# Optimization experiments

Hardware: AMD Instinct MI355X
Metric: run time of the kernel (lower is better)

The kernel has to match this reference:

```python
import jax, jax.numpy as jnp
import numpy as np

GROUP_SIZE = 128
IN_FEATURES = 8192
OUT_FEATURES = 28672
TOKENS = 32


def _dequantize(qweight, qzeros, scales):
    """ExLlama q4 dequant.
    qweight: (K//8, N) int32, 8 int4 values per word packed along k.
    qzeros:  (G, N//8) int32, 8 int4 zeros per word packed along n.
    scales:  (G, N) fp16.  g = k // GROUP_SIZE; w = s * (q - (z + 1)).
    """
    shifts = jnp.arange(8, dtype=jnp.int32) * 4
    K = qweight.shape[0] * 8
    N = qweight.shape[1]
    G = qzeros.shape[0]
    # unpack weights along k: (K//8, 8, N) -> (K, N)
    q = (qweight[:, None, :] >> shifts[None, :, None]) & 15
    q = q.reshape(K, N)
    # unpack zeros along n: (G, N//8, 8) -> (G, N)
    z = (qzeros[:, :, None] >> shifts[None, None, :]) & 15
    z = z.reshape(G, N)
    # group-wise dequant: reshape k into (G, GROUP_SIZE)
    qg = q.reshape(G, GROUP_SIZE, N).astype(jnp.float16)
    zf = (z + 1).astype(jnp.float16)[:, None, :]          # ExLlama stores zero-1
    w = (qg - zf) * scales[:, None, :]                    # (G, GS, N) fp16
    return w.reshape(K, N)


def setup_inputs() -> dict:
    key = jax.random.key(0)
    k1, k2, k3, k4, k5 = jax.random.split(key, 5)
    x = jax.random.normal(k1, (TOKENS, IN_FEATURES), dtype=jnp.float16)
    qweight = jax.random.randint(k2, (IN_FEATURES // 8, OUT_FEATURES),
                                 minval=-(2**31), maxval=2**31 - 1, dtype=jnp.int32)
    qzeros = jax.random.randint(k3, (IN_FEATURES // GROUP_SIZE, OUT_FEATURES // 8),
                                minval=-(2**31), maxval=2**31 - 1, dtype=jnp.int32)
    scales = (jax.random.uniform(k4, (IN_FEATURES // GROUP_SIZE, OUT_FEATURES),
                                 dtype=jnp.float32) * 0.01 + 0.001).astype(jnp.float16)
    bias = jax.random.normal(k5, (OUT_FEATURES,), dtype=jnp.float16)
    return {"x": x, "qweight": qweight, "qzeros": qzeros,
            "scales": scales, "bias": bias}


def reference(x, qweight, qzeros, scales, bias):
    w = _dequantize(qweight, qzeros, scales)              # (K, N) fp16
    out = jnp.matmul(x.astype(jnp.float16), w)            # (T, N)
    return out + bias
```

## Files before the change

kernel.cpp:

```cpp
#include <hip/hip_runtime.h>

#define T_TOK   32
#define KDIM    8192
#define NDIM    28672
#define NZW     3584
#define NSEG    16
#define SEGK    (KDIM / NSEG)
#define GPS     4
#define XIT     ((T_TOK * SEGK) / (256 * 8))

typedef _Float16 half8  __attribute__((ext_vector_type(8)));
typedef float    f32x4  __attribute__((ext_vector_type(4)));
typedef _Float16 half2v __attribute__((ext_vector_type(2)));
typedef unsigned uint4v __attribute__((ext_vector_type(4)));

template<bool ATOMIC>
__global__ __launch_bounds__(256)
void exllama_gemm16(const int*   __restrict__ qweight,
                    const int*   __restrict__ qzeros,
                    const float* __restrict__ scales,
                    const float* __restrict__ x,
                    const float* __restrict__ bias,
                    _Float16*    __restrict__ ws,
                    float*       __restrict__ out)
{
    __shared__ alignas(16) _Float16 xs[T_TOK * SEGK];
    char* xb = (char*)xs;

    const int tid  = threadIdx.x;
    const int lane = tid & 63;
    const int wav  = tid >> 6;
    const int quad = lane >> 4;
    const int l16  = lane & 15;
    const int seg  = blockIdx.y;
    const int n0   = blockIdx.x * 128 + wav * 32;
    const int g0   = seg * GPS;

    int nc[2];
    #pragma unroll
    for (int j = 0; j < 2; ++j) nc[j] = n0 + j * 16 + l16;

    unsigned qw[GPS][8];
    #pragma unroll
    for (int g = 0; g < GPS; ++g) {
        const size_t rb = (size_t)((g0 + g) * 16 + quad) * NDIM;
        #pragma unroll
        for (int c = 0; c < 4; ++c)
            #pragma unroll
            for (int j = 0; j < 2; ++j)
                qw[g][c * 2 + j] = (unsigned)qweight[rb + (size_t)(c * 4) * NDIM + nc[j]];
    }

    float sraw[GPS][2];
    int   zraw[GPS][2];
    #pragma unroll
    for (int g = 0; g < GPS; ++g)
        #pragma unroll
        for (int j = 0; j < 2; ++j) {
            sraw[g][j] = scales[(size_t)(g0 + g) * NDIM + nc[j]];
            zraw[g][j] = qzeros[(size_t)(g0 + g) * NZW + (nc[j] >> 3)];
        }

    {
        const int kseg0 = seg * SEGK;
        #pragma unroll
        for (int it = 0; it < XIT; ++it) {
            const int e  = it * 2048 + tid * 8;
            const int t  = e >> 9;
            const int kl = e & (SEGK - 1);
            const float* xp = x + (size_t)t * KDIM + kseg0 + kl;
            f32x4 lo = *(const f32x4*)xp;
            f32x4 hi = *(const f32x4*)(xp + 4);
            uint4v u;
            #pragma unroll
            for (int j = 0; j < 4; ++j)
                u[j] = __builtin_bit_cast(unsigned,
                          __builtin_amdgcn_cvt_pkrtz(lo[j], hi[j]));
            const int off = (t * 1024 + kl * 2) ^ ((t & 7) << 4);
            *(uint4v*)(xb + off) = u;
        }
    }

    half2v sp[GPS][2], cp[GPS][2];
    #pragma unroll
    for (int g = 0; g < GPS; ++g)
        #pragma unroll
        for (int j = 0; j < 2; ++j) {
            const int z = (zraw[g][j] >> ((nc[j] & 7) * 4)) & 15;
            const _Float16 sh = (_Float16)sraw[g][j];
            const _Float16 ch = (_Float16)(float)(-(1025 + z));
            sp[g][j] = (half2v){sh, sh};
            cp[g][j] = (half2v){ch, ch};
        }

    __syncthreads();

    f32x4 acc[2][2];
    #pragma unroll
    for (int j = 0; j < 2; ++j)
        #pragma unroll
        for (int m = 0; m < 2; ++m)
            acc[j][m] = (f32x4){0.f, 0.f, 0.f, 0.f};

    #pragma unroll
    for (int g = 0; g < GPS; ++g) {
        #pragma unroll
        for (int c = 0; c < 4; ++c) {
            const int kloc = g * 128 + c * 32 + quad * 8;
            const int o0 = (l16 * 1024 + kloc * 2) ^ ((l16 & 7) << 4);
            half8 a0 = *(const half8*)(xb + o0);
            half8 a1 = *(const half8*)(xb + o0 + 16 * 1024);
            #pragma unroll
            for (int j = 0; j < 2; ++j) {
                const unsigned w = qw[g][c * 2 + j];
                uint4v bu;
                #pragma unroll
                for (int i = 0; i < 4; ++i) {
                    unsigned t = ((w >> (4 * i)) & 0x000F000Fu) | 0x64006400u;
                    half2v th = __builtin_bit_cast(half2v, t);
                    half2v r  = (th + cp[g][j]) * sp[g][j];
                    bu[i] = __builtin_bit_cast(unsigned, r);
                }
                half8 bf = __builtin_bit_cast(half8, bu);
                acc[j][0] = __builtin_amdgcn_mfma_f32_16x16x32_f16(a0, bf, acc[j][0], 0, 0, 0);
                acc[j][1] = __builtin_amdgcn_mfma_f32_16x16x32_f16(a1, bf, acc[j][1], 0, 0, 0);
            }
        }
    }

    if (ATOMIC) {
        #pragma unroll
        for (int j = 0; j < 2; ++j) {
            const float bb = bias[nc[j]] * (1.0f / NSEG);
            #pragma unroll
            for (int m = 0; m < 2; ++m)
                #pragma unroll
                for (int r = 0; r < 4; ++r) {
                    const int t = m * 16 + quad * 4 + r;
                    unsafeAtomicAdd(out + (size_t)t * NDIM + nc[j], acc[j][m][r] + bb);
                }
        }
    } else {
        _Float16* wsp = ws + (size_t)seg * (T_TOK * NDIM);
        #pragma unroll
        for (int j = 0; j < 2; ++j)
            #pragma unroll
            for (int m = 0; m < 2; ++m)
                #pragma unroll
                for (int r = 0; r < 4; ++r) {
                    const int t = m * 16 + quad * 4 + r;
                    wsp[(size_t)t * NDIM + nc[j]] = (_Float16)acc[j][m][r];
                }
    }
}

__global__ __launch_bounds__(256)
void reduce_bias(const _Float16* __restrict__ ws,
                 const float*    __restrict__ bias,
                 float*          __restrict__ out)
{
    const int e = (blockIdx.x * 256 + threadIdx.x) * 8;
    const int n = e % NDIM;
    float sum[8] = {0.f, 0.f, 0.f, 0.f, 0.f, 0.f, 0.f, 0.f};
    #pragma unroll
    for (int s = 0; s < NSEG; ++s) {
        half8 v = *(const half8*)(ws + (size_t)s * (T_TOK * NDIM) + e);
        #pragma unroll
        for (int i = 0; i < 8; ++i) sum[i] += (float)v[i];
    }
    f32x4 o0, o1;
    #pragma unroll
    for (int i = 0; i < 4; ++i) {
        o0[i] = sum[i]     + bias[n + i];
        o1[i] = sum[i + 4] + bias[n + 4 + i];
    }
    *(f32x4*)(out + e)     = o0;
    *(f32x4*)(out + e + 4) = o1;
}

extern "C" void kernel_launch(void* const* d_in, const int* in_sizes, int n_in,
                              void* d_out, int out_size, void* d_ws, size_t ws_size,
                              hipStream_t stream)
{
    const float* x  = (const float*)d_in[0];
    const int* qweight = (const int*)d_in[1];
    const int* qzeros  = (const int*)d_in[2];
    const float* sc = (const float*)d_in[3];
    const float* bs = (const float*)d_in[4];
    float* out      = (float*)d_out;

    const size_t need = (size_t)NSEG * T_TOK * NDIM * sizeof(_Float16);
    if (ws_size >= need) {
        exllama_gemm16<false><<<dim3(NDIM / 128, NSEG), 256, 0, stream>>>(
            qweight, qzeros, sc, x, bs, (_Float16*)d_ws, out);
        reduce_bias<<<(T_TOK * NDIM) / (256 * 8), 256, 0, stream>>>(
            (const _Float16*)d_ws, bs, out);
    } else {
        exllama_gemm16<true><<<dim3(NDIM / 128, NSEG), 256, 0, stream>>>(
            qweight, qzeros, sc, x, bs, nullptr, out);
    }
}
```

Measured before the change: 198.3 us.

## Precompute fp16 activations once and read them directly from global memory

Adds a separate pre-pass kernel that converts x from fp32 to fp16 once into workspace. The GEMM kernel then drops its shared-memory staging and barrier and loads MFMA A-fragments straight from global memory (L2-resident), prefetching the next fragment one step ahead. This removes the per-block redundant conversion, the LDS traffic and the __syncthreads, which also frees LDS to allow higher occupancy. The cost is an extra kernel launch and uncoalesced, repeated global reads of x that depend on cache hits.

```diff
diff --git a/kernel.cpp b/kernel.cpp
--- a/kernel.cpp
+++ b/kernel.cpp
@@ -7,26 +7,36 @@
 #define NSEG    16
 #define SEGK    (KDIM / NSEG)
 #define GPS     4
-#define XIT     ((T_TOK * SEGK) / (256 * 8))
 
 typedef _Float16 half8  __attribute__((ext_vector_type(8)));
+typedef _Float16 half2v __attribute__((ext_vector_type(2)));
 typedef float    f32x4  __attribute__((ext_vector_type(4)));
-typedef _Float16 half2v __attribute__((ext_vector_type(2)));
 typedef unsigned uint4v __attribute__((ext_vector_type(4)));
 
-template<bool ATOMIC>
 __global__ __launch_bounds__(256)
-void exllama_gemm16(const int*   __restrict__ qweight,
-                    const int*   __restrict__ qzeros,
-                    const float* __restrict__ scales,
-                    const float* __restrict__ x,
-                    const float* __restrict__ bias,
-                    _Float16*    __restrict__ ws,
-                    float*       __restrict__ out)
-{
-    __shared__ alignas(16) _Float16 xs[T_TOK * SEGK];
-    char* xb = (char*)xs;
-
+void xprep(const float* __restrict__ x, _Float16* __restrict__ xp)
+{
+    const int idx = blockIdx.x * 256 + threadIdx.x;
+    const int t   = idx >> 10;
+    const int k0  = (idx & 1023) * 8;
+    const float* src = x + (size_t)t * KDIM + k0;
+    f32x4 lo = *(const f32x4*)src;
+    f32x4 hi = *(const f32x4*)(src + 4);
+    uint4v u;
+    #pragma unroll
+    for (int j = 0; j < 4; ++j)
+        u[j] = __builtin_bit_cast(unsigned,
+                  __builtin_amdgcn_cvt_pkrtz(lo[j], hi[j]));
+    *(uint4v*)(xp + (size_t)t * KDIM + k0) = u;
+}
+
+__global__ __launch_bounds__(256)
+void exllama_gemm_nolds(const int*      __restrict__ qweight,
+                        const int*      __restrict__ qzeros,
+                        const float*    __restrict__ scales,
+                        const _Float16* __restrict__ xp,
+                        _Float16*       __restrict__ ws)
+{
     const int tid  = threadIdx.x;
     const int lane = tid & 63;
     const int wav  = tid >> 6;
@@ -35,10 +45,11 @@
     const int seg  = blockIdx.y;
     const int n0   = blockIdx.x * 128 + wav * 32;
     const int g0   = seg * GPS;
+    const int kseg0 = seg * SEGK;
 
     int nc[2];
-    #pragma unroll
-    for (int j = 0; j < 2; ++j) nc[j] = n0 + j * 16 + l16;
+    nc[0] = n0 + l16;
+    nc[1] = n0 + 16 + l16;
 
     unsigned qw[GPS][8];
     #pragma unroll
@@ -61,25 +72,8 @@
             zraw[g][j] = qzeros[(size_t)(g0 + g) * NZW + (nc[j] >> 3)];
         }
 
-    {
-        const int kseg0 = seg * SEGK;
-        #pragma unroll
-        for (int it = 0; it < XIT; ++it) {
-            const int e  = it * 2048 + tid * 8;
-            const int t  = e >> 9;
-            const int kl = e & (SEGK - 1);
-            const float* xp = x + (size_t)t * KDIM + kseg0 + kl;
-            f32x4 lo = *(const f32x4*)xp;
-            f32x4 hi = *(const f32x4*)(xp + 4);
-            uint4v u;
-            #pragma unroll
-            for (int j = 0; j < 4; ++j)
-                u[j] = __builtin_bit_cast(unsigned,
-                          __builtin_amdgcn_cvt_pkrtz(lo[j], hi[j]));
-            const int off = (t * 1024 + kl * 2) ^ ((t & 7) << 4);
-            *(uint4v*)(xb + off) = u;
-        }
-    }
+    const _Float16* xr0 = xp + (size_t)l16 * KDIM + kseg0 + quad * 8;
+    const _Float16* xr1 = xr0 + (size_t)16 * KDIM;
 
     half2v sp[GPS][2], cp[GPS][2];
     #pragma unroll
@@ -93,8 +87,6 @@
             cp[g][j] = (half2v){ch, ch};
         }
 
-    __syncthreads();
-
     f32x4 acc[2][2];
     #pragma unroll
     for (int j = 0; j < 2; ++j)
@@ -102,6 +94,155 @@
         for (int m = 0; m < 2; ++m)
             acc[j][m] = (f32x4){0.f, 0.f, 0.f, 0.f};
 
+    half8 a0 = *(const half8*)(xr0);
+    half8 a1 = *(const half8*)(xr1);
+    #pragma unroll
+    for (int g = 0; g < GPS; ++g) {
+        #pragma unroll
+        for (int c = 0; c < 4; ++c) {
+            const half8 ca0 = a0;
+            const half8 ca1 = a1;
+            const int nx = g * 4 + c + 1;
+            if (nx < 16) {
+                const int kn = (nx >> 2) * 128 + (nx & 3) * 32;
+                a0 = *(const half8*)(xr0 + kn);
+                a1 = *(const half8*)(xr1 + kn);
+            }
+            #pragma unroll
+            for (int j = 0; j < 2; ++j) {
+                const unsigned w = qw[g][c * 2 + j];
+                uint4v bu;
+                #pragma unroll
+                for (int i = 0; i < 4; ++i) {
+                    unsigned t = ((w >> (4 * i)) & 0x000F000Fu) | 0x64006400u;
+                    half2v th = __builtin_bit_cast(half2v, t);
+                    half2v r  = (th + cp[g][j]) * sp[g][j];
+                    bu[i] = __builtin_bit_cast(unsigned, r);
+                }
+                half8 bf = __builtin_bit_cast(half8, bu);
+                acc[j][0] = __builtin_amdgcn_mfma_f32_16x16x32_f16(ca0, bf, acc[j][0], 0, 0, 0);
+                acc[j][1] = __builtin_amdgcn_mfma_f32_16x16x32_f16(ca1, bf, acc[j][1], 0, 0, 0);
+            }
+        }
+    }
+
+    _Float16* wsp = ws + (size_t)seg * (T_TOK * NDIM);
+    #pragma unroll
+    for (int j = 0; j < 2; ++j)
+        #pragma unroll
+        for (int m = 0; m < 2; ++m)
+            #pragma unroll
+            for (int r = 0; r < 4; ++r) {
+                const int t = m * 16 + quad * 4 + r;
+                wsp[(size_t)t * NDIM + nc[j]] = (_Float16)acc[j][m][r];
+            }
+}
+
+__global__ __launch_bounds__(256)
+void reduce_bias(const _Float16* __restrict__ ws,
+                 const float*    __restrict__ bias,
+                 float*          __restrict__ out)
+{
+    const int e = (blockIdx.x * 256 + threadIdx.x) * 8;
+    const int n = e % NDIM;
+    float sum[8] = {0.f, 0.f, 0.f, 0.f, 0.f, 0.f, 0.f, 0.f};
+    #pragma unroll
+    for (int s = 0; s < NSEG; ++s) {
+        half8 v = *(const half8*)(ws + (size_t)s * (T_TOK * NDIM) + e);
+        #pragma unroll
+        for (int i = 0; i < 8; ++i) sum[i] += (float)v[i];
+    }
+    f32x4 o0, o1;
+    #pragma unroll
+    for (int i = 0; i < 4; ++i) {
+        o0[i] = sum[i]     + bias[n + i];
+        o1[i] = sum[i + 4] + bias[n + 4 + i];
+    }
+    *(f32x4*)(out + e)     = o0;
+    *(f32x4*)(out + e + 4) = o1;
+}
+
+__global__ __launch_bounds__(256)
+void exllama_gemm_atomic(const int*   __restrict__ qweight,
+                         const int*   __restrict__ qzeros,
+                         const float* __restrict__ scales,
+                         const float* __restrict__ x,
+                         const float* __restrict__ bias,
+                         float*       __restrict__ out)
+{
+    __shared__ alignas(16) _Float16 xs[T_TOK * SEGK];
+    char* xb = (char*)xs;
+
+    const int tid  = threadIdx.x;
+    const int lane = tid & 63;
+    const int wav  = tid >> 6;
+    const int quad = lane >> 4;
+    const int l16  = lane & 15;
+    const int seg  = blockIdx.y;
+    const int n0   = blockIdx.x * 128 + wav * 32;
+    const int g0   = seg * GPS;
+
+    int nc[2];
+    nc[0] = n0 + l16;
+    nc[1] = n0 + 16 + l16;
+
+    unsigned qw[GPS][8];
+    #pragma unroll
+    for (int g = 0; g < GPS; ++g) {
+        const size_t rb = (size_t)((g0 + g) * 16 + quad) * NDIM;
+        #pragma unroll
+        for (int c = 0; c < 4; ++c)
+            #pragma unroll
+            for (int j = 0; j < 2; ++j)
+                qw[g][c * 2 + j] = (unsigned)qweight[rb + (size_t)(c * 4) * NDIM + nc[j]];
+    }
+    float sraw[GPS][2];
+    int   zraw[GPS][2];
+    #pragma unroll
+    for (int g = 0; g < GPS; ++g)
+        #pragma unroll
+        for (int j = 0; j < 2; ++j) {
+            sraw[g][j] = scales[(size_t)(g0 + g) * NDIM + nc[j]];
+            zraw[g][j] = qzeros[(size_t)(g0 + g) * NZW + (nc[j] >> 3)];
+        }
+    {
+        const int kseg0 = seg * SEGK;
+        #pragma unroll
+        for (int it = 0; it < 8; ++it) {
+            const int e  = it * 2048 + tid * 8;
+            const int t  = e >> 9;
+            const int kl = e & (SEGK - 1);
+            const float* xpr = x + (size_t)t * KDIM + kseg0 + kl;
+            f32x4 lo = *(const f32x4*)xpr;
+            f32x4 hi = *(const f32x4*)(xpr + 4);
+            uint4v u;
+            #pragma unroll
+            for (int j = 0; j < 4; ++j)
+                u[j] = __builtin_bit_cast(unsigned,
+                          __builtin_amdgcn_cvt_pkrtz(lo[j], hi[j]));
+            const int off = (t * 1024 + kl * 2) ^ ((t & 7) << 4);
+            *(uint4v*)(xb + off) = u;
+        }
+    }
+    half2v sp[GPS][2], cp[GPS][2];
+    #pragma unroll
+    for (int g = 0; g < GPS; ++g)
+        #pragma unroll
+        for (int j = 0; j < 2; ++j) {
+            const int z = (zraw[g][j] >> ((nc[j] & 7) * 4)) & 15;
+            const _Float16 sh = (_Float16)sraw[g][j];
+            const _Float16 ch = (_Float16)(float)(-(1025 + z));
+            sp[g][j] = (half2v){sh, sh};
+            cp[g][j] = (half2v){ch, ch};
+        }
+    __syncthreads();
+
+    f32x4 acc[2][2];
+    #pragma unroll
+    for (int j = 0; j < 2; ++j)
+        #pragma unroll
+        for (int m = 0; m < 2; ++m)
+            acc[j][m] = (f32x4){0.f, 0.f, 0.f, 0.f};
     #pragma unroll
     for (int g = 0; g < GPS; ++g) {
         #pragma unroll
@@ -127,55 +268,17 @@
             }
         }
     }
-
-    if (ATOMIC) {
-        #pragma unroll
-        for (int j = 0; j < 2; ++j) {
-            const float bb = bias[nc[j]] * (1.0f / NSEG);
-            #pragma unroll
-            for (int m = 0; m < 2; ++m)
-                #pragma unroll
-                for (int r = 0; r < 4; ++r) {
-                    const int t = m * 16 + quad * 4 + r;
-                    unsafeAtomicAdd(out + (size_t)t * NDIM + nc[j], acc[j][m][r] + bb);
-                }
-        }
-    } else {
-        _Float16* wsp = ws + (size_t)seg * (T_TOK * NDIM);
-        #pragma unroll
-        for (int j = 0; j < 2; ++j)
-            #pragma unroll
-            for (int m = 0; m < 2; ++m)
-                #pragma unroll
-                for (int r = 0; r < 4; ++r) {
-                    const int t = m * 16 + quad * 4 + r;
-                    wsp[(size_t)t * NDIM + nc[j]] = (_Float16)acc[j][m][r];
-                }
-    }
-}
-
-__global__ __launch_bounds__(256)
-void reduce_bias(const _Float16* __restrict__ ws,
-                 const float*    __restrict__ bias,
-                 float*          __restrict__ out)
-{
-    const int e = (blockIdx.x * 256 + threadIdx.x) * 8;
-    const int n = e % NDIM;
-    float sum[8] = {0.f, 0.f, 0.f, 0.f, 0.f, 0.f, 0.f, 0.f};
-    #pragma unroll
-    for (int s = 0; s < NSEG; ++s) {
-        half8 v = *(const half8*)(ws + (size_t)s * (T_TOK * NDIM) + e);
-        #pragma unroll
-        for (int i = 0; i < 8; ++i) sum[i] += (float)v[i];
-    }
-    f32x4 o0, o1;
-    #pragma unroll
-    for (int i = 0; i < 4; ++i) {
-        o0[i] = sum[i]     + bias[n + i];
-        o1[i] = sum[i + 4] + bias[n + 4 + i];
-    }
-    *(f32x4*)(out + e)     = o0;
-    *(f32x4*)(out + e + 4) = o1;
+    #pragma unroll
+    for (int j = 0; j < 2; ++j) {
+        const float bb = bias[nc[j]] * (1.0f / NSEG);
+        #pragma unroll
+        for (int m = 0; m < 2; ++m)
+            #pragma unroll
+            for (int r = 0; r < 4; ++r) {
+                const int t = m * 16 + quad * 4 + r;
+                unsafeAtomicAdd(out + (size_t)t * NDIM + nc[j], acc[j][m][r] + bb);
+            }
+    }
 }
 
 extern "C" void kernel_launch(void* const* d_in, const int* in_sizes, int n_in,
@@ -189,14 +292,18 @@
     const float* bs = (const float*)d_in[4];
     float* out      = (float*)d_out;
 
-    const size_t need = (size_t)NSEG * T_TOK * NDIM * sizeof(_Float16);
-    if (ws_size >= need) {
-        exllama_gemm16<false><<<dim3(NDIM / 128, NSEG), 256, 0, stream>>>(
-            qweight, qzeros, sc, x, bs, (_Float16*)d_ws, out);
+    const size_t xpbytes = (size_t)T_TOK * KDIM * sizeof(_Float16);
+    const size_t pbytes  = (size_t)NSEG * T_TOK * NDIM * sizeof(_Float16);
+    if (ws_size >= xpbytes + pbytes) {
+        _Float16* xp   = (_Float16*)d_ws;
+        _Float16* part = xp + (size_t)T_TOK * KDIM;
+        xprep<<<(T_TOK * KDIM / 8) / 256, 256, 0, stream>>>(x, xp);
+        exllama_gemm_nolds<<<dim3(NDIM / 128, NSEG), 256, 0, stream>>>(
+            qweight, qzeros, sc, xp, part);
         reduce_bias<<<(T_TOK * NDIM) / (256 * 8), 256, 0, stream>>>(
-            (const _Float16*)d_ws, bs, out);
+            part, bs, out);
     } else {
-        exllama_gemm16<true><<<dim3(NDIM / 128, NSEG), 256, 0, stream>>>(
-            qweight, qzeros, sc, x, bs, nullptr, out);
-    }
-}
+        exllama_gemm_atomic<<<dim3(NDIM / 128, NSEG), 256, 0, stream>>>(
+            qweight, qzeros, sc, x, bs, out);
+    }
+}
```

Result: slower. 226.2 us (+14.1%).
